# Optimization experiments

Measured on AMD Instinct MI355X. Metric: run time of the kernel, lower is better.

Reference implementation:

```python
import jax, jax.numpy as jnp
import numpy as np
from jax import lax

K_NEIGHBORS = 3  # n_neighbors


def _divide_no_nan(x, d):
    # tf.math.divide_no_nan semantics: 0 where denominator is 0
    safe = jnp.where(d == 0, 1.0, d)
    return jnp.where(d == 0, 0.0, x / safe)


def setup_inputs() -> dict:
    key = jax.random.key(0)
    k1, k2, k3 = jax.random.split(key, 3)
    B, N, D, C = 512, 200000, 27, 10
    queries = jax.random.normal(k1, (B, D), dtype=jnp.float32)
    features = jax.random.normal(k2, (N, D), dtype=jnp.float32)
    cls = jax.random.randint(k3, (N,), 0, C)
    labels = jax.nn.one_hot(cls, C, dtype=jnp.float32)
    return {"queries": queries, "features": features, "labels": labels}


def reference(queries, features, labels):
    # scale_tensor: per-dim max of |training features| (computed at init in the TF model)
    scale = jnp.max(jnp.abs(features), axis=0)              # (D,)
    fs = _divide_no_nan(features, scale)                    # (N, D)
    qs = _divide_no_nan(queries, scale)                     # (B, D)

    # pairwise Euclidean distances (B, N) == tf.norm(fs - q, axis=1) per query
    d2 = (jnp.sum(fs * fs, axis=1)[None, :]
          - 2.0 * qs @ fs.T
          + jnp.sum(qs * qs, axis=1)[:, None])
    dist = jnp.sqrt(jnp.maximum(d2, 0.0))                   # (B, N)

    neg_kd, idx = lax.top_k(-dist, K_NEIGHBORS)             # (B, K)
    kd = -neg_kd                                            # k smallest distances
    lab = labels[idx]                                       # (B, K, C) gather

    # weighted vote: sum_k label_k / dist_k, then argmax -> one-hot
    safe_kd = jnp.where(kd == 0, 1.0, kd)
    weighted = jnp.sum(lab / safe_kd[..., None], axis=1)    # (B, C)
    vote = jax.nn.one_hot(jnp.argmax(weighted, axis=-1), labels.shape[1],
                          dtype=labels.dtype)

    # exact-match branch: if min distance == 0, take nearest neighbor's label
    zero_hit = (jnp.min(kd, axis=1, keepdims=True) == 0)    # (B, 1)
    result = jnp.where(zero_hit, lab[:, 0, :], vote)        # (B, C)

    # concatenated (k_smallest_distances, result_tensor) per query: (B, K + C)
    return jnp.concatenate([kd, result], axis=-1)
```

## Files before the change

### kernel.cpp

```cpp
#include <hip/hip_runtime.h>
#include <math.h>

#define NQ     512
#define DD     27
#define NC     10
#define KK     3
#define NTHR   256
#define NSLICE 256
#define NBLK   (NSLICE*4)
#define NCAND  (NSLICE*3)

static __device__ __forceinline__ unsigned fbits(float x){ return __float_as_uint(x); }

__global__ void k_scale(const float* __restrict__ feats, unsigned* __restrict__ scale_bits,
                        int total, int total_f4) {
  __shared__ unsigned smax[DD];
  int t = threadIdx.x;
  if (t < DD) smax[t] = 0u;
  __syncthreads();
  int gid = blockIdx.x * blockDim.x + t;
  int stride = gridDim.x * blockDim.x;
  const float4* f4 = (const float4*)feats;
  float m0=0.f, m1=0.f, m2=0.f, m3=0.f;
  for (int i = gid; i < total_f4; i += stride) {
    float4 v = f4[i];
    m0 = fmaxf(m0, fabsf(v.x));
    m1 = fmaxf(m1, fabsf(v.y));
    m2 = fmaxf(m2, fabsf(v.z));
    m3 = fmaxf(m3, fabsf(v.w));
  }
  int d0 = (4*gid) % DD;
  atomicMax(&smax[d0],          fbits(m0));
  atomicMax(&smax[(d0+1)%DD],   fbits(m1));
  atomicMax(&smax[(d0+2)%DD],   fbits(m2));
  atomicMax(&smax[(d0+3)%DD],   fbits(m3));
  if (gid == 0) {
    for (int i = total_f4*4; i < total; ++i)
      atomicMax(&scale_bits[i % DD], fbits(fabsf(feats[i])));
  }
  __syncthreads();
  if (t < DD) atomicMax(&scale_bits[t], smax[t]);
}

__global__ void k_prep(const float* __restrict__ queries, const unsigned* __restrict__ scale_bits,
                       float* __restrict__ rscale, float* __restrict__ qp,
                       float* __restrict__ qnorm) {
  __shared__ float rs[DD];
  int t = threadIdx.x;
  if (t < DD) {
    float s = __uint_as_float(scale_bits[t]);
    float r = (s == 0.f) ? 0.f : 1.f / s;
    rs[t] = r;
    rscale[t] = r;
  }
  __syncthreads();
  float nrm = 0.f;
  #pragma unroll
  for (int d = 0; d < DD; ++d) {
    float v = queries[t*DD + d] * rs[d];
    qp[t*DD + d] = v * rs[d];
    nrm = fmaf(v, v, nrm);
  }
  qnorm[t] = nrm;
}

__global__ void k_fnorm(const float* __restrict__ feats, const float* __restrict__ rscale,
                        float* __restrict__ fnorm2, int nfeat) {
  __shared__ float rs[DD];
  int t = threadIdx.x;
  if (t < DD) rs[t] = rscale[t];
  __syncthreads();
  int f = blockIdx.x * blockDim.x + t;
  if (f < nfeat) {
    const float* row = feats + (size_t)f*DD;
    float acc = 0.f;
    #pragma unroll
    for (int d = 0; d < DD; ++d) { float v = row[d] * rs[d]; acc = fmaf(v, v, acc); }
    fnorm2[f] = acc;
  }
}

#define TINS(acc, fi, sA, sB, sC, iA, iB, iC) do {                        \
    if ((acc) > sC) {                                                     \
      if ((acc) > sA)      { sC=sB;iC=iB; sB=sA;iB=iA; sA=(acc);iA=(fi); }\
      else if ((acc) > sB) { sC=sB;iC=iB; sB=(acc);iB=(fi); }             \
      else                 { sC=(acc); iC=(fi); }                         \
    }                                                                     \
  } while (0)

#define DECLQ(d)  float q0_##d = qp[qa*DD + (d)]; float q1_##d = qp[(qa+64)*DD + (d)];
#define QF(d)     { float fv_ = row[d]; a0 = fmaf(fv_, q0_##d, a0); a1 = fmaf(fv_, q1_##d, a1); }

__global__ __launch_bounds__(NTHR, 4) void k_knn(
    const float* __restrict__ feats, const float* __restrict__ qp,
    const float* __restrict__ fnorm2, float* __restrict__ pd2v,
    int* __restrict__ pd2i, int nfeat) {
  int t = threadIdx.x;
  int lane = t & 63;
  int w = __builtin_amdgcn_readfirstlane(t >> 6);
  int b = blockIdx.x;
  int qt    = b >> 8;
  int slice = b & (NSLICE-1);

  int qa = qt*128 + lane;
  DECLQ(0)  DECLQ(1)  DECLQ(2)  DECLQ(3)  DECLQ(4)  DECLQ(5)  DECLQ(6)
  DECLQ(7)  DECLQ(8)  DECLQ(9)  DECLQ(10) DECLQ(11) DECLQ(12) DECLQ(13)
  DECLQ(14) DECLQ(15) DECLQ(16) DECLQ(17) DECLQ(18) DECLQ(19) DECLQ(20)
  DECLQ(21) DECLQ(22) DECLQ(23) DECLQ(24) DECLQ(25) DECLQ(26)
  asm volatile("" : "+v"(q0_0),"+v"(q0_1),"+v"(q0_2),"+v"(q0_3),"+v"(q0_4),
                    "+v"(q0_5),"+v"(q0_6),"+v"(q0_7),"+v"(q0_8),"+v"(q0_9),
                    "+v"(q0_10),"+v"(q0_11),"+v"(q0_12),"+v"(q0_13));
  asm volatile("" : "+v"(q0_14),"+v"(q0_15),"+v"(q0_16),"+v"(q0_17),"+v"(q0_18),
                    "+v"(q0_19),"+v"(q0_20),"+v"(q0_21),"+v"(q0_22),"+v"(q0_23),
                    "+v"(q0_24),"+v"(q0_25),"+v"(q0_26));
  asm volatile("" : "+v"(q1_0),"+v"(q1_1),"+v"(q1_2),"+v"(q1_3),"+v"(q1_4),
                    "+v"(q1_5),"+v"(q1_6),"+v"(q1_7),"+v"(q1_8),"+v"(q1_9),
                    "+v"(q1_10),"+v"(q1_11),"+v"(q1_12),"+v"(q1_13));
  asm volatile("" : "+v"(q1_14),"+v"(q1_15),"+v"(q1_16),"+v"(q1_17),"+v"(q1_18),
                    "+v"(q1_19),"+v"(q1_20),"+v"(q1_21),"+v"(q1_22),"+v"(q1_23),
                    "+v"(q1_24),"+v"(q1_25),"+v"(q1_26));

  float s00=-INFINITY, s01=-INFINITY, s02=-INFINITY;
  float s10=-INFINITY, s11=-INFINITY, s12=-INFINITY;
  int   i00=0x7fffffff, i01=0x7fffffff, i02=0x7fffffff;
  int   i10=0x7fffffff, i11=0x7fffffff, i12=0x7fffffff;

  int S = (nfeat + NSLICE - 1) / NSLICE;
  int base = slice * S;
  int cnt = nfeat - base; if (cnt > S) cnt = S; if (cnt < 0) cnt = 0;
  int fb = base + (cnt * w) / 4;
  int fe = base + (cnt * (w+1)) / 4;

  #pragma unroll 2
  for (int f = fb; f < fe; ++f) {
    const float* row = feats + (size_t)f * DD;
    float fn = fnorm2[f];
    float a0 = -0.5f * fn;
    float a1 = -0.5f * fn;
    QF(0)  QF(1)  QF(2)  QF(3)  QF(4)  QF(5)  QF(6)  QF(7)  QF(8)
    QF(9)  QF(10) QF(11) QF(12) QF(13) QF(14) QF(15) QF(16) QF(17)
    QF(18) QF(19) QF(20) QF(21) QF(22) QF(23) QF(24) QF(25) QF(26)
    TINS(a0, f, s00, s01, s02, i00, i01, i02);
    TINS(a1, f, s10, s11, s12, i10, i11, i12);
  }

  __shared__ float sv[4][128][3];
  __shared__ int   sx[4][128][3];
  sv[w][lane][0]    = s00; sv[w][lane][1]    = s01; sv[w][lane][2]    = s02;
  sx[w][lane][0]    = i00; sx[w][lane][1]    = i01; sx[w][lane][2]    = i02;
  sv[w][lane+64][0] = s10; sv[w][lane+64][1] = s11; sv[w][lane+64][2] = s12;
  sx[w][lane+64][0] = i10; sx[w][lane+64][1] = i11; sx[w][lane+64][2] = i12;
  __syncthreads();
  if (t < 128) {
    float b0=-INFINITY, b1=-INFINITY, b2=-INFINITY;
    int   x0=0x7fffffff, x1=0x7fffffff, x2=0x7fffffff;
    #pragma unroll
    for (int ww = 0; ww < 4; ++ww) {
      #pragma unroll
      for (int j = 0; j < 3; ++j) {
        float v = sv[ww][t][j]; int ix = sx[ww][t][j];
        if (v > b2 || (v == b2 && ix < x2)) {
          if (v > b0 || (v == b0 && ix < x0))      { b2=b1;x2=x1; b1=b0;x1=x0; b0=v;x0=ix; }
          else if (v > b1 || (v == b1 && ix < x1)) { b2=b1;x2=x1; b1=v;x1=ix; }
          else                                     { b2=v; x2=ix; }
        }
      }
    }
    int q = qt*128 + t;
    long o = (long)q * NCAND + slice*3;
    pd2v[o+0] = -2.f*b0; pd2v[o+1] = -2.f*b1; pd2v[o+2] = -2.f*b2;
    pd2i[o+0] = x0;      pd2i[o+1] = x1;      pd2i[o+2] = x2;
  }
}

#define INS(vv, ii) do { \
  if ((vv) < c2 || ((vv) == c2 && (ii) < j2)) { \
    if ((vv) < c0 || ((vv) == c0 && (ii) < j0))      { c2=c1;j2=j1; c1=c0;j1=j0; c0=(vv);j0=(ii); } \
    else if ((vv) < c1 || ((vv) == c1 && (ii) < j1)) { c2=c1;j2=j1; c1=(vv);j1=(ii); } \
    else                                             { c2=(vv); j2=(ii); } \
  } \
} while (0)

__global__ __launch_bounds__(NTHR) void k_merge(
    const float* __restrict__ pd2v, const int* __restrict__ pd2i,
    const float* __restrict__ qnorm, const float* __restrict__ labels,
    float* __restrict__ out) {
  __shared__ float sk[NTHR*3];
  __shared__ int   si[NTHR*3];
  int q = blockIdx.x, t = threadIdx.x;
  float c0=INFINITY, c1=INFINITY, c2=INFINITY;
  int   j0=0x7fffffff, j1=0x7fffffff, j2=0x7fffffff;
  const float* pv = pd2v + (long)q * NCAND;
  const int*   pi = pd2i + (long)q * NCAND;
  for (int i = t; i < NCAND; i += NTHR) {
    float v = pv[i]; int ix = pi[i];
    INS(v, ix);
  }
  sk[t*3+0]=c0; sk[t*3+1]=c1; sk[t*3+2]=c2;
  si[t*3+0]=j0; si[t*3+1]=j1; si[t*3+2]=j2;
  __syncthreads();
  if (t < 64) {
    for (int s = 1; s < 4; ++s) {
      int bb = t + s*64;
      #pragma unroll
      for (int k = 0; k < 3; ++k) { float v = sk[bb*3+k]; int ix = si[bb*3+k]; INS(v, ix); }
    }
    sk[t*3+0]=c0; sk[t*3+1]=c1; sk[t*3+2]=c2;
    si[t*3+0]=j0; si[t*3+1]=j1; si[t*3+2]=j2;
  }
  __syncthreads();
  if (t == 0) {
    for (int s = 1; s < 64; ++s) {
      #pragma unroll
      for (int k = 0; k < 3; ++k) { float v = sk[s*3+k]; int ix = si[s*3+k]; INS(v, ix); }
    }
    float qn = qnorm[q];
    float kd0 = sqrtf(fmaxf(c0 + qn, 0.f));
    float kd1 = sqrtf(fmaxf(c1 + qn, 0.f));
    float kd2 = sqrtf(fmaxf(c2 + qn, 0.f));
    const float* l0 = labels + (long)j0 * NC;
    const float* l1 = labels + (long)j1 * NC;
    const float* l2 = labels + (long)j2 * NC;
    float inv0 = 1.f / ((kd0 == 0.f) ? 1.f : kd0);
    float inv1 = 1.f / ((kd1 == 0.f) ? 1.f : kd1);
    float inv2 = 1.f / ((kd2 == 0.f) ? 1.f : kd2);
    float wv[NC];
    #pragma unroll
    for (int cc = 0; cc < NC; ++cc)
      wv[cc] = l0[cc]*inv0 + l1[cc]*inv1 + l2[cc]*inv2;
    int am = 0; float bw = wv[0];
    #pragma unroll
    for (int cc = 1; cc < NC; ++cc) if (wv[cc] > bw) { bw = wv[cc]; am = cc; }
    float* o = out + q * (KK + NC);
    o[0] = kd0; o[1] = kd1; o[2] = kd2;
    if (kd0 == 0.f) {
      #pragma unroll
      for (int cc = 0; cc < NC; ++cc) o[3+cc] = l0[cc];
    } else {
      #pragma unroll
      for (int cc = 0; cc < NC; ++cc) o[3+cc] = (cc == am) ? 1.f : 0.f;
    }
  }
}

extern "C" void kernel_launch(void* const* d_in, const int* in_sizes, int n_in,
                              void* d_out, int out_size, void* d_ws, size_t ws_size,
                              hipStream_t stream) {
  const float* queries = (const float*)d_in[0];
  const float* feats   = (const float*)d_in[1];
  const float* labels  = (const float*)d_in[2];
  float* out = (float*)d_out;
  char*  ws  = (char*)d_ws;

  int total = in_sizes[1];
  int nfeat = total / DD;

  unsigned* scale_bits = (unsigned*)ws;
  float* rscale = (float*)(ws + 256);
  float* qnorm  = (float*)(ws + 512);
  float* qp     = (float*)(ws + 4096);
  float* fnorm2 = (float*)(ws + 65536);
  float* pd2v   = (float*)(ws + 1048576);
  int*   pd2i   = (int*)(ws + 1048576 + 2097152);

  hipMemsetAsync(ws, 0, 128, stream);
  k_scale<<<864, 256, 0, stream>>>(feats, scale_bits, total, total / 4);
  k_prep <<<1, NQ, 0, stream>>>(queries, scale_bits, rscale, qp, qnorm);
  k_fnorm<<<(nfeat + 255) / 256, 256, 0, stream>>>(feats, rscale, fnorm2, nfeat);
  k_knn  <<<NBLK, NTHR, 0, stream>>>(feats, qp, fnorm2, pd2v, pd2i, nfeat);
  k_merge<<<NQ, NTHR, 0, stream>>>(pd2v, pd2i, qnorm, labels, out);
}
```

Baseline: 261.1 us.

## Repartition kNN so each block covers all queries over a feature slice

The kNN kernel now launches one block per feature slice (1024 slices), with each of its four waves holding 128 distinct queries. Previously each block covered a 128-query tile and split the slice across waves, then reduced through shared memory. Each feature row is now read once per block for all 512 queries instead of once per query tile, and the in-block merge is dropped. The cost is four times as many candidates for the merge kernel to scan, a larger candidate buffer, and a looser launch bound. The feature-norm kernel now stages rows through shared memory with coalesced loads and recomputes the reciprocal scale itself, so the separate rscale buffer is gone.

Result: slower. 292.7 us (+12.1%).

```diff
diff --git a/kernel.cpp b/kernel.cpp
--- a/kernel.cpp
+++ b/kernel.cpp
@@ -6,8 +6,7 @@
 #define NC     10
 #define KK     3
 #define NTHR   256
-#define NSLICE 256
-#define NBLK   (NSLICE*4)
+#define NSLICE 1024
 #define NCAND  (NSLICE*3)
 
 static __device__ __forceinline__ unsigned fbits(float x){ return __float_as_uint(x); }
@@ -43,15 +42,12 @@
 }
 
 __global__ void k_prep(const float* __restrict__ queries, const unsigned* __restrict__ scale_bits,
-                       float* __restrict__ rscale, float* __restrict__ qp,
-                       float* __restrict__ qnorm) {
+                       float* __restrict__ qp, float* __restrict__ qnorm) {
   __shared__ float rs[DD];
   int t = threadIdx.x;
   if (t < DD) {
     float s = __uint_as_float(scale_bits[t]);
-    float r = (s == 0.f) ? 0.f : 1.f / s;
-    rs[t] = r;
-    rscale[t] = r;
+    rs[t] = (s == 0.f) ? 0.f : 1.f / s;
   }
   __syncthreads();
   float nrm = 0.f;
@@ -64,45 +60,58 @@
   qnorm[t] = nrm;
 }
 
-__global__ void k_fnorm(const float* __restrict__ feats, const float* __restrict__ rscale,
-                        float* __restrict__ fnorm2, int nfeat) {
+__global__ __launch_bounds__(NTHR) void k_fnorm(
+    const float* __restrict__ feats, const unsigned* __restrict__ scale_bits,
+    float* __restrict__ fnorm2, int nfeat) {
   __shared__ float rs[DD];
-  int t = threadIdx.x;
-  if (t < DD) rs[t] = rscale[t];
-  __syncthreads();
-  int f = blockIdx.x * blockDim.x + t;
+  __shared__ float rows[NTHR*DD];
+  int t = threadIdx.x;
+  if (t < DD) {
+    float s = __uint_as_float(scale_bits[t]);
+    rs[t] = (s == 0.f) ? 0.f : 1.f / s;
+  }
+  __syncthreads();
+  int fbase = blockIdx.x * NTHR;
+  int gbase = fbase * DD;
+  int ntot  = nfeat * DD;
+  #pragma unroll
+  for (int j = 0; j < DD; ++j) {
+    int idx = t + j*NTHR;
+    int g = gbase + idx;
+    rows[idx] = (g < ntot) ? feats[g] : 0.f;
+  }
+  __syncthreads();
+  int f = fbase + t;
   if (f < nfeat) {
-    const float* row = feats + (size_t)f*DD;
     float acc = 0.f;
     #pragma unroll
-    for (int d = 0; d < DD; ++d) { float v = row[d] * rs[d]; acc = fmaf(v, v, acc); }
+    for (int d = 0; d < DD; ++d) { float v = rows[t*DD + d] * rs[d]; acc = fmaf(v, v, acc); }
     fnorm2[f] = acc;
   }
 }
 
-#define TINS(acc, fi, sA, sB, sC, iA, iB, iC) do {                        \
-    if ((acc) > sC) {                                                     \
-      if ((acc) > sA)      { sC=sB;iC=iB; sB=sA;iB=iA; sA=(acc);iA=(fi); }\
-      else if ((acc) > sB) { sC=sB;iC=iB; sB=(acc);iB=(fi); }             \
-      else                 { sC=(acc); iC=(fi); }                         \
+#define TINS(acc, fi, s0, s1, s2, i0, i1, i2) do {                        \
+    if ((acc) > s2) {                                                     \
+      if ((acc) > s0)      { s2=s1;i2=i1; s1=s0;i1=i0; s0=(acc);i0=(fi); }\
+      else if ((acc) > s1) { s2=s1;i2=i1; s1=(acc);i1=(fi); }             \
+      else                 { s2=(acc); i2=(fi); }                         \
     }                                                                     \
   } while (0)
 
-#define DECLQ(d)  float q0_##d = qp[qa*DD + (d)]; float q1_##d = qp[(qa+64)*DD + (d)];
+#define DECLQ(d)  float q0_##d = qp[q0i*DD + (d)]; float q1_##d = qp[q1i*DD + (d)];
 #define QF(d)     { float fv_ = row[d]; a0 = fmaf(fv_, q0_##d, a0); a1 = fmaf(fv_, q1_##d, a1); }
 
-__global__ __launch_bounds__(NTHR, 4) void k_knn(
+__global__ __launch_bounds__(NTHR) void k_knn(
     const float* __restrict__ feats, const float* __restrict__ qp,
     const float* __restrict__ fnorm2, float* __restrict__ pd2v,
     int* __restrict__ pd2i, int nfeat) {
   int t = threadIdx.x;
   int lane = t & 63;
-  int w = __builtin_amdgcn_readfirstlane(t >> 6);
-  int b = blockIdx.x;
-  int qt    = b >> 8;
-  int slice = b & (NSLICE-1);
-
-  int qa = qt*128 + lane;
+  int w = t >> 6;
+  int slice = blockIdx.x;
+
+  int q0i = w*128 + lane;
+  int q1i = q0i + 64;
   DECLQ(0)  DECLQ(1)  DECLQ(2)  DECLQ(3)  DECLQ(4)  DECLQ(5)  DECLQ(6)
   DECLQ(7)  DECLQ(8)  DECLQ(9)  DECLQ(10) DECLQ(11) DECLQ(12) DECLQ(13)
   DECLQ(14) DECLQ(15) DECLQ(16) DECLQ(17) DECLQ(18) DECLQ(19) DECLQ(20)
@@ -120,6 +129,8 @@
                     "+v"(q1_19),"+v"(q1_20),"+v"(q1_21),"+v"(q1_22),"+v"(q1_23),
                     "+v"(q1_24),"+v"(q1_25),"+v"(q1_26));
 
+  __syncthreads();
+
   float s00=-INFINITY, s01=-INFINITY, s02=-INFINITY;
   float s10=-INFINITY, s11=-INFINITY, s12=-INFINITY;
   int   i00=0x7fffffff, i01=0x7fffffff, i02=0x7fffffff;
@@ -128,11 +139,9 @@
   int S = (nfeat + NSLICE - 1) / NSLICE;
   int base = slice * S;
   int cnt = nfeat - base; if (cnt > S) cnt = S; if (cnt < 0) cnt = 0;
-  int fb = base + (cnt * w) / 4;
-  int fe = base + (cnt * (w+1)) / 4;
-
-  #pragma unroll 2
-  for (int f = fb; f < fe; ++f) {
+  int fe = base + cnt;
+
+  for (int f = base; f < fe; ++f) {
     const float* row = feats + (size_t)f * DD;
     float fn = fnorm2[f];
     float a0 = -0.5f * fn;
@@ -144,33 +153,12 @@
     TINS(a1, f, s10, s11, s12, i10, i11, i12);
   }
 
-  __shared__ float sv[4][128][3];
-  __shared__ int   sx[4][128][3];
-  sv[w][lane][0]    = s00; sv[w][lane][1]    = s01; sv[w][lane][2]    = s02;
-  sx[w][lane][0]    = i00; sx[w][lane][1]    = i01; sx[w][lane][2]    = i02;
-  sv[w][lane+64][0] = s10; sv[w][lane+64][1] = s11; sv[w][lane+64][2] = s12;
-  sx[w][lane+64][0] = i10; sx[w][lane+64][1] = i11; sx[w][lane+64][2] = i12;
-  __syncthreads();
-  if (t < 128) {
-    float b0=-INFINITY, b1=-INFINITY, b2=-INFINITY;
-    int   x0=0x7fffffff, x1=0x7fffffff, x2=0x7fffffff;
-    #pragma unroll
-    for (int ww = 0; ww < 4; ++ww) {
-      #pragma unroll
-      for (int j = 0; j < 3; ++j) {
-        float v = sv[ww][t][j]; int ix = sx[ww][t][j];
-        if (v > b2 || (v == b2 && ix < x2)) {
-          if (v > b0 || (v == b0 && ix < x0))      { b2=b1;x2=x1; b1=b0;x1=x0; b0=v;x0=ix; }
-          else if (v > b1 || (v == b1 && ix < x1)) { b2=b1;x2=x1; b1=v;x1=ix; }
-          else                                     { b2=v; x2=ix; }
-        }
-      }
-    }
-    int q = qt*128 + t;
-    long o = (long)q * NCAND + slice*3;
-    pd2v[o+0] = -2.f*b0; pd2v[o+1] = -2.f*b1; pd2v[o+2] = -2.f*b2;
-    pd2i[o+0] = x0;      pd2i[o+1] = x1;      pd2i[o+2] = x2;
-  }
+  long o0 = (long)q0i * NCAND + slice*3;
+  pd2v[o0+0] = -2.f*s00; pd2v[o0+1] = -2.f*s01; pd2v[o0+2] = -2.f*s02;
+  pd2i[o0+0] = i00;      pd2i[o0+1] = i01;      pd2i[o0+2] = i02;
+  long o1 = (long)q1i * NCAND + slice*3;
+  pd2v[o1+0] = -2.f*s10; pd2v[o1+1] = -2.f*s11; pd2v[o1+2] = -2.f*s12;
+  pd2i[o1+0] = i10;      pd2i[o1+1] = i11;      pd2i[o1+2] = i12;
 }
 
 #define INS(vv, ii) do { \
@@ -256,17 +244,16 @@
   int nfeat = total / DD;
 
   unsigned* scale_bits = (unsigned*)ws;
-  float* rscale = (float*)(ws + 256);
   float* qnorm  = (float*)(ws + 512);
   float* qp     = (float*)(ws + 4096);
   float* fnorm2 = (float*)(ws + 65536);
   float* pd2v   = (float*)(ws + 1048576);
-  int*   pd2i   = (int*)(ws + 1048576 + 2097152);
+  int*   pd2i   = (int*)(ws + 8388608);
 
   hipMemsetAsync(ws, 0, 128, stream);
   k_scale<<<864, 256, 0, stream>>>(feats, scale_bits, total, total / 4);
-  k_prep <<<1, NQ, 0, stream>>>(queries, scale_bits, rscale, qp, qnorm);
-  k_fnorm<<<(nfeat + 255) / 256, 256, 0, stream>>>(feats, rscale, fnorm2, nfeat);
-  k_knn  <<<NBLK, NTHR, 0, stream>>>(feats, qp, fnorm2, pd2v, pd2i, nfeat);
+  k_prep <<<1, NQ, 0, stream>>>(queries, scale_bits, qp, qnorm);
+  k_fnorm<<<(nfeat + NTHR - 1) / NTHR, NTHR, 0, stream>>>(feats, scale_bits, fnorm2, nfeat);
+  k_knn  <<<NSLICE, NTHR, 0, stream>>>(feats, qp, fnorm2, pd2v, pd2i, nfeat);
   k_merge<<<NQ, NTHR, 0, stream>>>(pd2v, pd2i, qnorm, labels, out);
 }
```
